# Performance work log

Hardware: AMD Instinct MI355X
Metric: run time of the kernel (lower is better)

The kernel has to match this reference:

```python
import jax, jax.numpy as jnp
from jax import lax
import numpy as np
import math

# ---- static hyperparameters (from init_kwargs) ----
NUM_RAY = 64
NUM_RAY2 = NUM_RAY * NUM_RAY
NUM_SAMPLE = 64
STEP = 1.0 / (NUM_SAMPLE - 1)
RK = 3                       # RK4Range: neighbor cube side
K = 64                       # Num_RIGuassKernel per axis
PH = (192, 192, 192)         # PhantomSize (D, H, W)
THETA_X, THETA_Y, THETA_Z = 0.1, 0.05, 0.02
CENTER = (0.5, 0.5, 0.5)

# ---- constant neighbor offsets and kernel-center grids (Process_Parameter) ----
half = (RK - 1) // 2
_r = np.arange(-half, half + 1)
Xr_np, Yr_np, Zr_np = np.meshgrid(_r, _r, _r)
XR = jnp.asarray(Xr_np.flatten().reshape(1, RK ** 3), dtype=jnp.float32)
YR = jnp.asarray(Yr_np.flatten().reshape(1, RK ** 3), dtype=jnp.float32)
ZR = jnp.asarray(Zr_np.flatten().reshape(1, RK ** 3), dtype=jnp.float32)
_c = np.linspace(0, 1, K, dtype='float32')
Xc_np, Yc_np, Zc_np = np.meshgrid(_c, _c, _c)
XC = jnp.asarray(Xc_np.flatten())
YC = jnp.asarray(Yc_np.flatten())
ZC = jnp.asarray(Zc_np.flatten())

# ---- rotation matrices (Theta2TransMatrix) ----
def _build_transmats():
    def ry(t):
        c, s = math.cos(t), math.sin(t)
        return np.array([[1, 0, 0, 0], [0, c, -s, 0], [0, s, c, 0], [0, 0, 0, 1]], dtype=np.float64)
    def rx(t):
        c, s = math.cos(t), math.sin(t)
        return np.array([[c, 0, -s, 0], [0, 1, 0, 0], [s, 0, c, 0], [0, 0, 0, 1]], dtype=np.float64)
    def rz(t):
        c, s = math.cos(t), math.sin(t)
        return np.array([[c, -s, 0, 0], [s, c, 0, 0], [0, 0, 1, 0], [0, 0, 0, 1]], dtype=np.float64)
    RY, RY_ = ry(-THETA_Y), ry(THETA_Y)
    RX, RX_ = rx(THETA_X), rx(-THETA_X)
    RZ, RZ_ = rz(-THETA_Z), rz(THETA_Z)
    cx, cy, cz = CENTER
    S1 = np.eye(4); S1[3, :3] = [-cx, -cy, -cz]
    S2 = np.eye(4); S2[3, :3] = [cx, cy, cz]
    M_crd = S1 @ RZ @ RY @ RX @ S2
    M_drv = RX_ @ RY_ @ RZ_
    return jnp.asarray(M_crd, dtype=jnp.float32), jnp.asarray(M_drv, dtype=jnp.float32)

M_CRD, M_DRV = _build_transmats()


def _indexdist(x, y, z, RI):
    # x,y,z: [N]; RI: [K^3, 2] -> Gaussian-kernel interpolated n and spatial derivatives
    X, Y, Z = x[:, None], y[:, None], z[:, None]
    Xn = jnp.clip(jnp.round(X * K) + XR, 0.0, K - 1.0)
    Yn = jnp.clip(jnp.round(Y * K) + YR, 0.0, K - 1.0)
    Zn = jnp.clip(jnp.round(Z * K) + ZR, 0.0, K - 1.0)
    lin = (K * K * Yn + K * Xn + Zn).astype(jnp.int32)   # [N, RK^3]
    dx = XC[lin] - X
    dy = YC[lin] - Y
    dz = ZC[lin] - Z
    A = RI[lin, 0]
    sig = RI[lin, 1]
    inv_s2 = 1.0 / (sig * sig)
    ni = jnp.exp(-(dx * dx + dy * dy + dz * dz) * 0.5 * inv_s2) + 2e-7
    norm = jnp.sum(ni, axis=1)
    nu = ni * A
    nx = jnp.sum(nu * dx * inv_s2, axis=1)
    ny = jnp.sum(nu * dy * inv_s2, axis=1)
    nz = jnp.sum(nu * dz * inv_s2, axis=1)
    ndx = jnp.sum(ni * dx * inv_s2, axis=1)
    ndy = jnp.sum(ni * dy * inv_s2, axis=1)
    ndz = jnp.sum(ni * dz * inv_s2, axis=1)
    nu_s = jnp.sum(nu, axis=1)
    n = nu_s / norm
    inv_norm2 = 1.0 / (norm * norm)
    nx = (norm * nx - nu_s * ndx) * inv_norm2
    ny = (norm * ny - nu_s * ndy) * inv_norm2
    nz = (norm * nz - nu_s * ndz) * inv_norm2
    return n, nx, ny, nz


def _rayeq(z0, xy0, RI):
    ones = jnp.ones_like(z0)
    t = jnp.stack([xy0[:, 2], xy0[:, 0], z0, ones], axis=1) @ M_CRD
    n, dndx_, dndy_, dndz_ = _indexdist(t[:, 1], t[:, 0], t[:, 2], RI)
    d = jnp.stack([dndy_, dndx_, dndz_, ones], axis=1) @ M_DRV
    dndx, dndz, dndy = d[:, 1], d[:, 2], d[:, 0]
    dX1 = xy0[:, 1]
    dX2 = (dndx - dndz * dX1) * (1.0 + dX1 * dX1) / n
    dY1 = xy0[:, 3]
    dY2 = (dndy - dndz * dY1) * (1.0 + dY1 * dY1) / n
    return jnp.stack([dX1, dX2, dY1, dY2], axis=1)


def _ray_tracing(xyz0, RI):
    def step_fn(xyz, _):
        deriv = _rayeq(xyz[:, 4], xyz[:, 0:4], RI)
        xyzi = jnp.concatenate([xyz[:, 0:4] + deriv * STEP, (xyz[:, 4] + STEP)[:, None]], axis=1)
        return xyzi, xyzi
    _, rest = lax.scan(step_fn, xyz0, None, length=NUM_SAMPLE - 1)
    return jnp.concatenate([xyz0[None], rest], axis=0)   # [S, N, 5]


def _resize_axis_linear(a, axis, out_len):
    # align_corners=True 1D linear resize along `axis`
    in_len = a.shape[axis]
    pos = jnp.linspace(0.0, in_len - 1.0, out_len)
    i0 = jnp.clip(jnp.floor(pos).astype(jnp.int32), 0, in_len - 2)
    w = (pos - i0.astype(pos.dtype)).astype(a.dtype)
    a0 = jnp.take(a, i0, axis=axis)
    a1 = jnp.take(a, i0 + 1, axis=axis)
    shape = [1] * a.ndim
    shape[axis] = out_len
    w = w.reshape(shape)
    return a0 * (1.0 - w) + a1 * w


def _grid_sample_3d(vol, gx, gy, gz):
    # torch F.grid_sample trilinear, align_corners=True, padding_mode='zeros'
    D, H, W = vol.shape
    ix = (gx + 1.0) * 0.5 * (W - 1)
    iy = (gy + 1.0) * 0.5 * (H - 1)
    iz = (gz + 1.0) * 0.5 * (D - 1)
    x0 = jnp.floor(ix); y0 = jnp.floor(iy); z0 = jnp.floor(iz)
    fx = ix - x0; fy = iy - y0; fz = iz - z0
    out = jnp.zeros_like(ix)
    for dz in (0, 1):
        for dyy in (0, 1):
            for dxx in (0, 1):
                xi = x0 + dxx; yi = y0 + dyy; zi = z0 + dz
                wgt = (jnp.where(dxx == 1, fx, 1.0 - fx)
                       * jnp.where(dyy == 1, fy, 1.0 - fy)
                       * jnp.where(dz == 1, fz, 1.0 - fz))
                inb = ((xi >= 0) & (xi <= W - 1) & (yi >= 0) & (yi <= H - 1)
                       & (zi >= 0) & (zi <= D - 1))
                xc = jnp.clip(xi, 0, W - 1).astype(jnp.int32)
                yc = jnp.clip(yi, 0, H - 1).astype(jnp.int32)
                zc = jnp.clip(zi, 0, D - 1).astype(jnp.int32)
                out = out + jnp.where(inb, wgt * vol[zc, yc, xc], 0.0)
    return out


def setup_inputs() -> dict:
    key = jax.random.key(0)
    k1, k2, k3, k4, k5 = jax.random.split(key, 5)
    Phantom = jax.random.uniform(k1, (1, 1) + PH, dtype=jnp.float32)
    A = jax.random.uniform(k2, (K ** 3, 1), dtype=jnp.float32) * 0.9 + 0.1
    sig = jax.random.uniform(k3, (K ** 3, 1), dtype=jnp.float32) * 0.8 + 0.2
    RefractionIndex = jnp.concatenate([A, sig], axis=1)
    xy = jax.random.uniform(k4, (NUM_RAY2, 2), dtype=jnp.float32) * 0.8 + 0.1
    slopes = jax.random.normal(k5, (NUM_RAY2, 2), dtype=jnp.float32) * 0.05
    z0 = jnp.zeros((NUM_RAY2, 1), dtype=jnp.float32)
    # layout [x, dx/dz, y, dy/dz, z]
    RayInit = jnp.concatenate([xy[:, :1], slopes[:, :1], xy[:, 1:], slopes[:, 1:], z0], axis=1)
    return {"Phantom": Phantom, "RefractionIndex": RefractionIndex, "RayInit": RayInit}


def reference(Phantom, RefractionIndex, RayInit):
    RayInit = RayInit.reshape(NUM_RAY2, 5)
    RI = RefractionIndex.reshape(K ** 3, 2)
    paths = _ray_tracing(RayInit, RI)          # [S, N, 5]
    paths = paths * 2.0 - 1.0
    # paths -> [3, R, R, S] mesh of (x, y, z) coordinates
    mesh = jnp.stack([
        paths[:, :, 0].T.reshape(NUM_RAY, NUM_RAY, NUM_SAMPLE),
        paths[:, :, 2].T.reshape(NUM_RAY, NUM_RAY, NUM_SAMPLE),
        paths[:, :, 4].T.reshape(NUM_RAY, NUM_RAY, NUM_SAMPLE),
    ], axis=0)
    # trilinear resize (align_corners=True) to PhantomSize
    for ax, out_len in zip((1, 2, 3), PH):
        mesh = _resize_axis_linear(mesh, ax, out_len)   # [3, D, H, W]
    vol = Phantom.reshape(PH)
    out = _grid_sample_3d(vol, mesh[0], mesh[1], mesh[2])
    return out.reshape((1, 1) + PH)
```

## Files before the change

kernel.cpp:

```cpp
#include <hip/hip_runtime.h>
#include <math.h>

#define NRAY2 4096
#define NSAMP 64
#define PHD 192
#define PLANE (PHD*PHD)
constexpr float STEP = 1.0f / 63.0f;

struct Mats { float crd[16]; float drv[16]; };

static void mat_mul4(const double* A, const double* B, double* C) {
    for (int i = 0; i < 4; ++i)
        for (int j = 0; j < 4; ++j) {
            double s = 0.0;
            for (int k = 0; k < 4; ++k) s += A[i*4+k] * B[k*4+j];
            C[i*4+j] = s;
        }
}

static void build_mats(Mats& M) {
    const double tx = 0.1, ty = 0.05, tz = 0.02;
    const double cx = 0.5, cy = 0.5, cz = 0.5;
    auto ry = [](double t, double* m) {
        double c = cos(t), s = sin(t);
        double v[16] = {1,0,0,0, 0,c,-s,0, 0,s,c,0, 0,0,0,1};
        for (int i = 0; i < 16; ++i) m[i] = v[i];
    };
    auto rx = [](double t, double* m) {
        double c = cos(t), s = sin(t);
        double v[16] = {c,0,-s,0, 0,1,0,0, s,0,c,0, 0,0,0,1};
        for (int i = 0; i < 16; ++i) m[i] = v[i];
    };
    auto rz = [](double t, double* m) {
        double c = cos(t), s = sin(t);
        double v[16] = {c,-s,0,0, s,c,0,0, 0,0,1,0, 0,0,0,1};
        for (int i = 0; i < 16; ++i) m[i] = v[i];
    };
    double RY[16], RY_[16], RX[16], RX_[16], RZ[16], RZ_[16];
    ry(-ty, RY); ry(ty, RY_);
    rx(tx, RX);  rx(-tx, RX_);
    rz(-tz, RZ); rz(tz, RZ_);
    double S1[16] = {1,0,0,0, 0,1,0,0, 0,0,1,0, -cx,-cy,-cz,1};
    double S2[16] = {1,0,0,0, 0,1,0,0, 0,0,1,0,  cx, cy, cz,1};
    double t1[16], t2[16], t3[16], Mc[16], Md[16];
    mat_mul4(S1, RZ, t1);
    mat_mul4(t1, RY, t2);
    mat_mul4(t2, RX, t3);
    mat_mul4(t3, S2, Mc);
    mat_mul4(RX_, RY_, t1);
    mat_mul4(t1, RZ_, Md);
    for (int i = 0; i < 16; ++i) { M.crd[i] = (float)Mc[i]; M.drv[i] = (float)Md[i]; }
}

template<int CTRL>
__device__ __forceinline__ void dpp_level8(float* v) {
    int t[8];
    #pragma unroll
    for (int i = 0; i < 8; ++i)
        t[i] = __builtin_amdgcn_update_dpp(0, __float_as_int(v[i]), CTRL, 0xF, 0xF, true);
    #pragma unroll
    for (int i = 0; i < 8; ++i) v[i] += __int_as_float(t[i]);
}

__device__ __forceinline__ void red8_16(float* v) {
    dpp_level8<0x121>(v);
    dpp_level8<0x122>(v);
    dpp_level8<0x124>(v);
    dpp_level8<0x128>(v);
}

__global__ __launch_bounds__(256) void ray_trace_kernel(
    const float* __restrict__ RI,
    const float* __restrict__ RayInit,
    float* __restrict__ meshXT,
    float* __restrict__ meshYT,
    Mats M)
{
    const int tid = threadIdx.x;
    const int nb  = tid & 15;
    const int ray = blockIdx.x * 16 + (tid >> 4);
    const bool act2 = nb < 11;

    const int n1 = nb, n2 = nb + 16;
    const float xr1 = (float)((n1/3)%3 - 1), yr1 = (float)(n1/9 - 1), zr1 = (float)(n1%3 - 1);
    const float xr2 = (float)((n2/3)%3 - 1), yr2 = (float)(n2/9 - 1), zr2 = (float)(n2%3 - 1);

    float X  = RayInit[ray*5 + 0];
    float dX = RayInit[ray*5 + 1];
    float Y  = RayInit[ray*5 + 2];
    float dY = RayInit[ray*5 + 3];
    float z  = RayInit[ray*5 + 4];

    if (nb == 0) meshXT[ray] = X*2.0f - 1.0f;
    if (nb == 1) meshYT[ray] = Y*2.0f - 1.0f;

    auto prep = [&](float pX, float pY, float pz,
                    float& ox, float& oy, float& oz,
                    float& X1, float& Y1, float& Z1,
                    float& X2, float& Y2, float& Z2,
                    float2& r1, float2& r2) {
        float x  = pY*M.crd[1] + pX*M.crd[5] + pz*M.crd[9]  + M.crd[13];
        float y  = pY*M.crd[0] + pX*M.crd[4] + pz*M.crd[8]  + M.crd[12];
        float zz = pY*M.crd[2] + pX*M.crd[6] + pz*M.crd[10] + M.crd[14];
        float rx_ = rintf(x*64.0f), ry_ = rintf(y*64.0f), rz_ = rintf(zz*64.0f);
        X1 = __builtin_amdgcn_fmed3f(rx_ + xr1, 0.0f, 63.0f);
        Y1 = __builtin_amdgcn_fmed3f(ry_ + yr1, 0.0f, 63.0f);
        Z1 = __builtin_amdgcn_fmed3f(rz_ + zr1, 0.0f, 63.0f);
        X2 = __builtin_amdgcn_fmed3f(rx_ + xr2, 0.0f, 63.0f);
        Y2 = __builtin_amdgcn_fmed3f(ry_ + yr2, 0.0f, 63.0f);
        Z2 = __builtin_amdgcn_fmed3f(rz_ + zr2, 0.0f, 63.0f);
        int l1 = (int)(Y1*4096.0f + X1*64.0f + Z1);
        int l2 = (int)(Y2*4096.0f + X2*64.0f + Z2);
        r1 = ((const float2*)RI)[l1];
        r2 = ((const float2*)RI)[l2];
        ox = x; oy = y; oz = zz;
    };

    float cx_, cy_, cz_, Xn1, Yn1, Zn1, Xn2, Yn2, Zn2;
    float2 ri1, ri2;
    prep(X, Y, z, cx_, cy_, cz_, Xn1, Yn1, Zn1, Xn2, Yn2, Zn2, ri1, ri2);

    const float C = -0.72134752044448169f;

    #pragma unroll 3
    for (int s = 1; s < NSAMP; ++s) {
        float nX = X + dX*STEP, nY = Y + dY*STEP, nz = z + STEP;
        float ncx, ncy, ncz, mX1, mY1, mZ1, mX2, mY2, mZ2;
        float2 ri1n, ri2n;
        prep(nX, nY, nz, ncx, ncy, ncz, mX1, mY1, mZ1, mX2, mY2, mZ2, ri1n, ri2n);

        float dx1 = Xn1*(1.0f/63.0f) - cx_;
        float dy1 = Yn1*(1.0f/63.0f) - cy_;
        float dz1 = Zn1*(1.0f/63.0f) - cz_;
        float is1 = __builtin_amdgcn_rcpf(ri1.y * ri1.y);
        float d21 = dx1*dx1 + dy1*dy1 + dz1*dz1;
        float e1  = __builtin_amdgcn_exp2f(d21 * is1 * C) + 2e-7f;
        float g1x = dx1*is1, g1y = dy1*is1, g1z = dz1*is1;
        float nu1 = e1 * ri1.x;

        float dx2 = Xn2*(1.0f/63.0f) - cx_;
        float dy2 = Yn2*(1.0f/63.0f) - cy_;
        float dz2 = Zn2*(1.0f/63.0f) - cz_;
        float is2 = __builtin_amdgcn_rcpf(ri2.y * ri2.y);
        float d22 = dx2*dx2 + dy2*dy2 + dz2*dz2;
        float e2  = __builtin_amdgcn_exp2f(d22 * is2 * C) + 2e-7f;
        if (!act2) e2 = 0.0f;
        float g2x = dx2*is2, g2y = dy2*is2, g2z = dz2*is2;
        float nu2 = e2 * ri2.x;

        float v[8] = { e1 + e2,
                       nu1 + nu2,
                       nu1*g1x + nu2*g2x,
                       nu1*g1y + nu2*g2y,
                       nu1*g1z + nu2*g2z,
                       e1*g1x + e2*g2x,
                       e1*g1y + e2*g2y,
                       e1*g1z + e2*g2z };
        red8_16(v);
        float ni  = v[0], nuA = v[1];
        float sx  = v[2], sy  = v[3], sz  = v[4];
        float sdx = v[5], sdy = v[6], sdz = v[7];

        float r   = __builtin_amdgcn_rcpf(ni);
        float rn  = ni * __builtin_amdgcn_rcpf(nuA);
        float in2 = r * r;
        float gx_ = (ni*sx - nuA*sdx) * in2;
        float gy_ = (ni*sy - nuA*sdy) * in2;
        float gz_ = (ni*sz - nuA*sdz) * in2;

        float dndx = gy_*M.drv[1] + gx_*M.drv[5] + gz_*M.drv[9]  + M.drv[13];
        float dndy = gy_*M.drv[0] + gx_*M.drv[4] + gz_*M.drv[8]  + M.drv[12];
        float dndz = gy_*M.drv[2] + gx_*M.drv[6] + gz_*M.drv[10] + M.drv[14];

        float dX2 = (dndx - dndz*dX) * (1.0f + dX*dX) * rn;
        float dY2 = (dndy - dndz*dY) * (1.0f + dY*dY) * rn;

        X = nX; Y = nY; z = nz;
        dX += dX2 * STEP;
        dY += dY2 * STEP;

        if (nb == 0) meshXT[s*NRAY2 + ray] = X*2.0f - 1.0f;
        if (nb == 1) meshYT[s*NRAY2 + ray] = Y*2.0f - 1.0f;

        cx_ = ncx; cy_ = ncy; cz_ = ncz;
        Xn1 = mX1; Yn1 = mY1; Zn1 = mZ1;
        Xn2 = mX2; Yn2 = mY2; Zn2 = mZ2;
        ri1 = ri1n; ri2 = ri2n;
    }
}

typedef _Float16 h16;
typedef _Float16 h16v4 __attribute__((ext_vector_type(4)));

__global__ __launch_bounds__(1024) void sample_kernel(
    const float* __restrict__ vol,
    const float* __restrict__ meshXT,
    const float* __restrict__ meshYT,
    h16*   __restrict__ outTh,
    float* __restrict__ outDirect,
    int transposed)
{
    __shared__ h16    plane_h[PLANE];
    __shared__ float2 slice[64*64];
    __shared__ float  wTab[PHD];
    __shared__ int    iTab[PHD];

    const int tid = threadIdx.x;
    const int blk = blockIdx.x;
    const int c = (blk >> 3) + 24 * (blk & 7);

    if (tid < PHD) {
        float p = tid * (63.0f / 191.0f);
        int i0 = min((int)p, 62);
        iTab[tid] = i0;
        wTab[tid] = p - (float)i0;
    }

    {
        const float4* src = (const float4*)(vol + c * PLANE);
        h16v4* dst = (h16v4*)plane_h;
        #pragma unroll
        for (int k = 0; k < (PLANE/4)/1024; ++k) {
            float4 v = src[tid + k*1024];
            h16v4 hv = {(h16)v.x, (h16)v.y, (h16)v.z, (h16)v.w};
            dst[tid + k*1024] = hv;
        }
    }

    float ps = c * (63.0f / 191.0f);
    int s0 = min((int)ps, 62);
    float wc = ps - (float)s0, wc0 = 1.0f - wc;
    {
        const float* x0 = meshXT + s0*NRAY2;
        const float* x1 = meshXT + (s0+1)*NRAY2;
        const float* y0 = meshYT + s0*NRAY2;
        const float* y1 = meshYT + (s0+1)*NRAY2;
        #pragma unroll
        for (int k = 0; k < 4096/1024; ++k) {
            int t = tid + k*1024;
            slice[t] = make_float2(x0[t]*wc0 + x1[t]*wc,
                                   y0[t]*wc0 + y1[t]*wc);
        }
    }
    __syncthreads();

    int a = tid / PHD, b = tid % PHD;
    #pragma unroll 4
    for (int k = 0; k < PLANE/1024; ++k) {
        int i0 = iTab[a]; float wa = wTab[a];
        int j0 = iTab[b]; float wb = wTab[b];

        float2 s00 = slice[i0*64 + j0];
        float2 s01 = slice[i0*64 + j0 + 1];
        float2 s10 = slice[(i0+1)*64 + j0];
        float2 s11 = slice[(i0+1)*64 + j0 + 1];

        float wb0 = 1.0f - wb, wa0 = 1.0f - wa;
        float gx = (s00.x*wb0 + s01.x*wb)*wa0 + (s10.x*wb0 + s11.x*wb)*wa;
        float gy = (s00.y*wb0 + s01.y*wb)*wa0 + (s10.y*wb0 + s11.y*wb)*wa;

        float ix = (gx + 1.0f) * 0.5f * 191.0f;
        float iy = (gy + 1.0f) * 0.5f * 191.0f;
        float x0f = floorf(ix); float fx = ix - x0f;
        float y0f = floorf(iy); float fy = iy - y0f;

        float acc = 0.0f;
        #pragma unroll
        for (int dyy = 0; dyy < 2; ++dyy) {
            #pragma unroll
            for (int dxx = 0; dxx < 2; ++dxx) {
                float xi = x0f + (float)dxx;
                float yi = y0f + (float)dyy;
                bool inb = (xi >= 0.0f) && (xi <= 191.0f) &&
                           (yi >= 0.0f) && (yi <= 191.0f);
                int xc = min(max((int)xi, 0), PHD - 1);
                int yc = min(max((int)yi, 0), PHD - 1);
                float w = (dxx ? fx : 1.0f - fx) * (dyy ? fy : 1.0f - fy);
                float val = (float)plane_h[yc*PHD + xc];
                acc += inb ? w * val : 0.0f;
            }
        }

        if (transposed) {
            outTh[c*PLANE + tid + k*1024] = (h16)acc;
        } else {
            outDirect[(a*PHD + b)*PHD + c] = acc;
        }

        a += 5; b += 64;
        if (b >= PHD) { b -= PHD; a += 1; }
    }
}

__global__ __launch_bounds__(256) void transpose_kernel(
    const h16* __restrict__ outTh, float* __restrict__ out)
{
    __shared__ h16 t[64][66];
    const int a  = blockIdx.z;
    const int b0 = blockIdx.x * 64;
    const int c0 = blockIdx.y * 64;
    const int tx = threadIdx.x & 63;
    const int ty = threadIdx.x >> 6;

    const h16* src = outTh + (size_t)(c0 + ty) * PLANE + a*PHD + b0 + tx;
    #pragma unroll
    for (int j = 0; j < 16; ++j)
        t[ty + 4*j][tx] = src[(size_t)(4*j) * PLANE];
    __syncthreads();

    float* dst = out + (size_t)a * PLANE + (size_t)(b0 + ty) * PHD + c0 + tx;
    #pragma unroll
    for (int j = 0; j < 16; ++j)
        dst[(size_t)(4*j) * PHD] = (float)t[tx][ty + 4*j];
}

extern "C" void kernel_launch(void* const* d_in, const int* in_sizes, int n_in,
                              void* d_out, int out_size, void* d_ws, size_t ws_size,
                              hipStream_t stream)
{
    const float* Phantom = (const float*)d_in[0];
    const float* RI      = (const float*)d_in[1];
    const float* RayInit = (const float*)d_in[2];
    float* out = (float*)d_out;

    float* meshXT = (float*)d_ws;
    float* meshYT = meshXT + NRAY2 * NSAMP;
    h16*   outTh  = (h16*)(meshYT + NRAY2 * NSAMP);

    const size_t need = (size_t)(2 * NRAY2 * NSAMP) * sizeof(float)
                      + (size_t)PHD * PLANE * sizeof(h16);
    const int use_transpose = (ws_size >= need) ? 1 : 0;

    Mats M;
    build_mats(M);

    ray_trace_kernel<<<NRAY2/16, 256, 0, stream>>>(RI, RayInit, meshXT, meshYT, M);

    if (use_transpose) {
        sample_kernel<<<PHD, 1024, 0, stream>>>(Phantom, meshXT, meshYT,
                                                outTh, nullptr, 1);
        transpose_kernel<<<dim3(3, 3, PHD), 256, 0, stream>>>(outTh, out);
    } else {
        sample_kernel<<<PHD, 1024, 0, stream>>>(Phantom, meshXT, meshYT,
                                                nullptr, out, 0);
    }
}
```

Before: 151.9 us.

## Process four outputs per thread in sampler, shrink ray-trace blocks

The sample kernel now has each thread handle four consecutive output columns. It loads six slice entries once, interpolates along the row axis once, and reuses the results for all four outputs. Outputs are written as a single vector store of four halves, and the shared lookup tables are replaced by inline arithmetic. Separately, the ray-trace kernel moves from 256-thread to 64-thread blocks with four rays each, giving 1024 blocks to spread better across CUs. The cost is more registers per thread in the sampler and less latency hiding from unrolling.

```diff
diff --git a/kernel.cpp b/kernel.cpp
--- a/kernel.cpp
+++ b/kernel.cpp
@@ -69,7 +69,7 @@
     dpp_level8<0x128>(v);
 }
 
-__global__ __launch_bounds__(256) void ray_trace_kernel(
+__global__ __launch_bounds__(64) void ray_trace_kernel(
     const float* __restrict__ RI,
     const float* __restrict__ RayInit,
     float* __restrict__ meshXT,
@@ -78,7 +78,7 @@
 {
     const int tid = threadIdx.x;
     const int nb  = tid & 15;
-    const int ray = blockIdx.x * 16 + (tid >> 4);
+    const int ray = blockIdx.x * 4 + (tid >> 4);
     const bool act2 = nb < 11;
 
     const int n1 = nb, n2 = nb + 16;
@@ -202,19 +202,12 @@
 {
     __shared__ h16    plane_h[PLANE];
     __shared__ float2 slice[64*64];
-    __shared__ float  wTab[PHD];
-    __shared__ int    iTab[PHD];
 
     const int tid = threadIdx.x;
     const int blk = blockIdx.x;
     const int c = (blk >> 3) + 24 * (blk & 7);
 
-    if (tid < PHD) {
-        float p = tid * (63.0f / 191.0f);
-        int i0 = min((int)p, 62);
-        iTab[tid] = i0;
-        wTab[tid] = p - (float)i0;
-    }
+    const float D = 63.0f / 191.0f;
 
     {
         const float4* src = (const float4*)(vol + c * PLANE);
@@ -227,9 +220,9 @@
         }
     }
 
-    float ps = c * (63.0f / 191.0f);
+    float ps = c * D;
     int s0 = min((int)ps, 62);
-    float wc = ps - (float)s0, wc0 = 1.0f - wc;
+    float wcs = ps - (float)s0, wc0 = 1.0f - wcs;
     {
         const float* x0 = meshXT + s0*NRAY2;
         const float* x1 = meshXT + (s0+1)*NRAY2;
@@ -238,57 +231,84 @@
         #pragma unroll
         for (int k = 0; k < 4096/1024; ++k) {
             int t = tid + k*1024;
-            slice[t] = make_float2(x0[t]*wc0 + x1[t]*wc,
-                                   y0[t]*wc0 + y1[t]*wc);
+            slice[t] = make_float2(x0[t]*wc0 + x1[t]*wcs,
+                                   y0[t]*wc0 + y1[t]*wcs);
         }
     }
     __syncthreads();
 
-    int a = tid / PHD, b = tid % PHD;
-    #pragma unroll 4
-    for (int k = 0; k < PLANE/1024; ++k) {
-        int i0 = iTab[a]; float wa = wTab[a];
-        int j0 = iTab[b]; float wb = wTab[b];
-
-        float2 s00 = slice[i0*64 + j0];
-        float2 s01 = slice[i0*64 + j0 + 1];
-        float2 s10 = slice[(i0+1)*64 + j0];
-        float2 s11 = slice[(i0+1)*64 + j0 + 1];
-
-        float wb0 = 1.0f - wb, wa0 = 1.0f - wa;
-        float gx = (s00.x*wb0 + s01.x*wb)*wa0 + (s10.x*wb0 + s11.x*wb)*wa;
-        float gy = (s00.y*wb0 + s01.y*wb)*wa0 + (s10.y*wb0 + s11.y*wb)*wa;
-
-        float ix = (gx + 1.0f) * 0.5f * 191.0f;
-        float iy = (gy + 1.0f) * 0.5f * 191.0f;
-        float x0f = floorf(ix); float fx = ix - x0f;
-        float y0f = floorf(iy); float fy = iy - y0f;
-
-        float acc = 0.0f;
+    #pragma unroll 1
+    for (int k = 0; k < PLANE/4096; ++k) {
+        const int w0 = (tid + k*1024) * 4;
+        const int a  = w0 / PHD;
+        const int b0 = w0 - a*PHD;
+
+        float pa = (float)a * D;
+        int   i0 = min((int)pa, 62);
+        float wa = pa - (float)i0;
+
+        float pb0 = (float)b0 * D;
+        int  jmin = min((int)pb0, 62);
+        int  j2   = min(jmin + 2, 63);
+
+        float2 r0c0 = slice[i0*64 + jmin];
+        float2 r0c1 = slice[i0*64 + jmin + 1];
+        float2 r0c2 = slice[i0*64 + j2];
+        float2 r1c0 = slice[(i0+1)*64 + jmin];
+        float2 r1c1 = slice[(i0+1)*64 + jmin + 1];
+        float2 r1c2 = slice[(i0+1)*64 + j2];
+
+        float c0x = r0c0.x + wa*(r1c0.x - r0c0.x);
+        float c0y = r0c0.y + wa*(r1c0.y - r0c0.y);
+        float c1x = r0c1.x + wa*(r1c1.x - r0c1.x);
+        float c1y = r0c1.y + wa*(r1c1.y - r0c1.y);
+        float c2x = r0c2.x + wa*(r1c2.x - r0c2.x);
+        float c2y = r0c2.y + wa*(r1c2.y - r0c2.y);
+
+        h16v4 res;
         #pragma unroll
-        for (int dyy = 0; dyy < 2; ++dyy) {
+        for (int m = 0; m < 4; ++m) {
+            float pb = (float)(b0 + m) * D;
+            int   j0 = min((int)pb, 62);
+            float wb = pb - (float)j0;
+            bool  hi = (j0 != jmin);
+
+            float sax = hi ? c1x : c0x, say = hi ? c1y : c0y;
+            float sbx = hi ? c2x : c1x, sby = hi ? c2y : c1y;
+            float gx = sax + wb*(sbx - sax);
+            float gy = say + wb*(sby - say);
+
+            float ix = (gx + 1.0f) * 0.5f * 191.0f;
+            float iy = (gy + 1.0f) * 0.5f * 191.0f;
+            float x0f = floorf(ix); float fx = ix - x0f;
+            float y0f = floorf(iy); float fy = iy - y0f;
+
+            float acc = 0.0f;
             #pragma unroll
-            for (int dxx = 0; dxx < 2; ++dxx) {
-                float xi = x0f + (float)dxx;
-                float yi = y0f + (float)dyy;
-                bool inb = (xi >= 0.0f) && (xi <= 191.0f) &&
-                           (yi >= 0.0f) && (yi <= 191.0f);
-                int xc = min(max((int)xi, 0), PHD - 1);
-                int yc = min(max((int)yi, 0), PHD - 1);
-                float w = (dxx ? fx : 1.0f - fx) * (dyy ? fy : 1.0f - fy);
-                float val = (float)plane_h[yc*PHD + xc];
-                acc += inb ? w * val : 0.0f;
+            for (int dyy = 0; dyy < 2; ++dyy) {
+                #pragma unroll
+                for (int dxx = 0; dxx < 2; ++dxx) {
+                    float xi = x0f + (float)dxx;
+                    float yi = y0f + (float)dyy;
+                    bool inb = (xi >= 0.0f) && (xi <= 191.0f) &&
+                               (yi >= 0.0f) && (yi <= 191.0f);
+                    int xc = min(max((int)xi, 0), PHD - 1);
+                    int yc = min(max((int)yi, 0), PHD - 1);
+                    float w = (dxx ? fx : 1.0f - fx) * (dyy ? fy : 1.0f - fy);
+                    float val = (float)plane_h[yc*PHD + xc];
+                    acc += inb ? w * val : 0.0f;
+                }
             }
+            res[m] = (h16)acc;
         }
 
         if (transposed) {
-            outTh[c*PLANE + tid + k*1024] = (h16)acc;
+            *(h16v4*)(outTh + (size_t)c*PLANE + w0) = res;
         } else {
-            outDirect[(a*PHD + b)*PHD + c] = acc;
-        }
-
-        a += 5; b += 64;
-        if (b >= PHD) { b -= PHD; a += 1; }
+            #pragma unroll
+            for (int m = 0; m < 4; ++m)
+                outDirect[(size_t)(a*PHD + b0 + m)*PHD + c] = (float)res[m];
+        }
     }
 }
 
@@ -334,7 +354,7 @@
     Mats M;
     build_mats(M);
 
-    ray_trace_kernel<<<NRAY2/16, 256, 0, stream>>>(RI, RayInit, meshXT, meshYT, M);
+    ray_trace_kernel<<<NRAY2/4, 64, 0, stream>>>(RI, RayInit, meshXT, meshYT, M);
 
     if (use_transpose) {
         sample_kernel<<<PHD, 1024, 0, stream>>>(Phantom, meshXT, meshYT,
```

Result: faster. 148.4 us (-2.3%).
